# Performance work log

Hardware: AMD Instinct MI355X
Metric: run time of the kernel (lower is better)

Reference implementation:

```python
import jax, jax.numpy as jnp
import numpy as np

B, S, H = 2, 2048, 2048
N_HEADS = 16
HEAD_DIM = H // N_HEADS


def setup_inputs() -> dict:
    key = jax.random.key(0)
    ks = jax.random.split(key, 9)
    s = 1.0 / np.sqrt(H)
    inp = {
        "x": jax.random.normal(ks[0], (B, S, H), dtype=jnp.float32),
        "wq": jax.random.uniform(ks[1], (H, H), jnp.float32, -s, s),
        "bq": jnp.zeros((H,), jnp.float32),
        "wk": jax.random.uniform(ks[2], (H, H), jnp.float32, -s, s),
        "bk": jnp.zeros((H,), jnp.float32),
        "wv": jax.random.uniform(ks[3], (H, H), jnp.float32, -s, s),
        "bv": jnp.zeros((H,), jnp.float32),
        "wo": jax.random.uniform(ks[4], (H, H), jnp.float32, -s, s),
        "bo": jnp.zeros((H,), jnp.float32),
    }
    return inp


def reference(x, wq, bq, wk, bk, wv, bv, wo, bo):
    bsz, seq_len, hidden = x.shape
    scale = HEAD_DIM ** -0.5
    # projections -> [b, h, s, d]
    def proj(w, b):
        y = jnp.einsum("bsh,oh->bso", x, w) + b
        return y.reshape(bsz, seq_len, N_HEADS, HEAD_DIM).transpose(0, 2, 1, 3)
    q = proj(wq, bq)
    k = proj(wk, bk)
    v = proj(wv, bv)
    scores = jnp.einsum("bhqd,bhkd->bhqk", q, k) * scale
    causal = jnp.tril(jnp.ones((seq_len, seq_len), dtype=bool))
    scores = jnp.where(causal, scores, -jnp.inf)
    attn = jax.nn.softmax(scores, axis=-1)
    out = jnp.einsum("bhqk,bhkd->bhqd", attn, v)
    out = out.transpose(0, 2, 1, 3).reshape(bsz, seq_len, hidden)
    return jnp.einsum("bsh,oh->bso", out, wo) + bo
```

## Files before the change

kernel.cpp:

```cpp
#include <hip/hip_runtime.h>
#include <hip/hip_bf16.h>
#include <cstdint>
#include <cstddef>

#define BATCH 2
#define S_LEN 2048
#define HID   2048
#define NH    16
#define HD    128
#define ATT_TILES (32 * NH * BATCH)

typedef short bf16x8 __attribute__((ext_vector_type(8)));
typedef float f32x4  __attribute__((ext_vector_type(4)));

__device__ inline unsigned short f2bf(float f) {
    unsigned int u = __float_as_uint(f);
    unsigned int r = (u + 0x7fffu + ((u >> 16) & 1u)) >> 16;
    return (unsigned short)r;
}

__global__ __launch_bounds__(256) void conv_f32_bf16(const float* __restrict__ src,
                                                     unsigned short* __restrict__ dst,
                                                     long n) {
    long i = ((long)blockIdx.x * 256 + threadIdx.x) * 8;
    if (i >= n) return;
    const float4 a = *(const float4*)(src + i);
    const float4 b = *(const float4*)(src + i + 4);
    union { unsigned short u[8]; bf16x8 v; } o;
    o.u[0] = f2bf(a.x); o.u[1] = f2bf(a.y); o.u[2] = f2bf(a.z); o.u[3] = f2bf(a.w);
    o.u[4] = f2bf(b.x); o.u[5] = f2bf(b.y); o.u[6] = f2bf(b.z); o.u[7] = f2bf(b.w);
    *(bf16x8*)(dst + i) = o.v;
}

__global__ __launch_bounds__(256) void conv4_f32_bf16(const float* __restrict__ s0,
                                                      const float* __restrict__ s1,
                                                      const float* __restrict__ s2,
                                                      const float* __restrict__ s3,
                                                      unsigned short* __restrict__ d0,
                                                      unsigned short* __restrict__ d1,
                                                      unsigned short* __restrict__ d2,
                                                      unsigned short* __restrict__ d3,
                                                      long n) {
    const int z = blockIdx.y;
    const float* src = (z == 0) ? s0 : (z == 1) ? s1 : (z == 2) ? s2 : s3;
    unsigned short* dst = (z == 0) ? d0 : (z == 1) ? d1 : (z == 2) ? d2 : d3;
    long i = ((long)blockIdx.x * 256 + threadIdx.x) * 8;
    if (i >= n) return;
    const float4 a = *(const float4*)(src + i);
    const float4 b = *(const float4*)(src + i + 4);
    union { unsigned short u[8]; bf16x8 v; } o;
    o.u[0] = f2bf(a.x); o.u[1] = f2bf(a.y); o.u[2] = f2bf(a.z); o.u[3] = f2bf(a.w);
    o.u[4] = f2bf(b.x); o.u[5] = f2bf(b.y); o.u[6] = f2bf(b.z); o.u[7] = f2bf(b.w);
    *(bf16x8*)(dst + i) = o.v;
}

__global__ void zero_int(int* p) { *p = 0; }

__device__ __forceinline__ void gemm_core(const unsigned short* __restrict__ A,
                                          const unsigned short* __restrict__ Bw,
                                          const float* __restrict__ bias,
                                          void* __restrict__ Cout,
                                          int M, int N, int K, int mode,
                                          int m0, int n0,
                                          unsigned short* Sm) {
    unsigned short* As = Sm;
    unsigned short* Bs = Sm + 4096;
    const int tid = threadIdx.x;
    const int lane = tid & 63;
    const int wave = tid >> 6;
    const int g = lane >> 4, ln = lane & 15;
    const int wm = (wave & 1) * 64, wn = (wave >> 1) * 64;

    f32x4 acc[4][4];
#pragma unroll
    for (int i = 0; i < 4; ++i)
#pragma unroll
        for (int j = 0; j < 4; ++j) acc[i][j] = (f32x4){0.f, 0.f, 0.f, 0.f};

    const int srow = wave * 16 + (lane >> 2);
    const int scol = (((lane & 3) ^ ((lane >> 3) & 3)) * 8);
    const int rxor = (ln >> 1) & 3;

    for (int k0 = 0; k0 < K; k0 += 32) {
#pragma unroll
        for (int c = 0; c < 2; ++c) {
            const unsigned short* ga = A  + (size_t)(m0 + c * 64 + srow) * K + k0 + scol;
            const unsigned short* gb = Bw + (size_t)(n0 + c * 64 + srow) * K + k0 + scol;
            __builtin_amdgcn_global_load_lds(
                (const __attribute__((address_space(1))) void*)ga,
                (__attribute__((address_space(3))) void*)(As + c * 2048 + wave * 512),
                16, 0, 0);
            __builtin_amdgcn_global_load_lds(
                (const __attribute__((address_space(1))) void*)gb,
                (__attribute__((address_space(3))) void*)(Bs + c * 2048 + wave * 512),
                16, 0, 0);
        }
        __syncthreads();
        bf16x8 af[4], bfr[4];
#pragma unroll
        for (int t = 0; t < 4; ++t) {
            af[t]  = *(const bf16x8*)&As[(wm + t * 16 + ln) * 32 + (g ^ rxor) * 8];
            bfr[t] = *(const bf16x8*)&Bs[(wn + t * 16 + ln) * 32 + (g ^ rxor) * 8];
        }
#pragma unroll
        for (int mt = 0; mt < 4; ++mt)
#pragma unroll
            for (int nt = 0; nt < 4; ++nt)
                acc[mt][nt] = __builtin_amdgcn_mfma_f32_16x16x32_bf16(af[mt], bfr[nt], acc[mt][nt], 0, 0, 0);
        __syncthreads();
    }

    if (mode == 1) {
        const int b = m0 >> 11;
        const int sbase = m0 & 2047;
        const int h = n0 >> 7;
#pragma unroll
        for (int p2 = 0; p2 < 2; ++p2) {
            if ((wave >> 1) == p2) {
#pragma unroll
                for (int nt = 0; nt < 4; ++nt) {
                    const int dl = nt * 16 + ln;
                    const float bn = bias[n0 + p2 * 64 + dl];
#pragma unroll
                    for (int mt = 0; mt < 4; ++mt)
#pragma unroll
                        for (int r = 0; r < 4; ++r) {
                            const int sl = wm + mt * 16 + g * 4 + r;
                            const int psc = (sl >> 3) ^ (dl & 15);
                            Sm[dl * 128 + psc * 8 + (sl & 7)] = f2bf(acc[mt][nt][r] + bn);
                        }
                }
            }
            __syncthreads();
            const int dl = tid >> 2;
            const int dd = p2 * 64 + dl;
            unsigned short* dst = (unsigned short*)Cout +
                ((size_t)(b * NH + h) * HD + dd) * S_LEN + sbase;
#pragma unroll
            for (int j = 0; j < 4; ++j) {
                const int sc = (tid & 3) * 4 + j;
                const int psc = sc ^ (dl & 15);
                *(bf16x8*)(dst + sc * 8) = *(const bf16x8*)&Sm[dl * 128 + psc * 8];
            }
            __syncthreads();
        }
        return;
    }

#pragma unroll
    for (int mt = 0; mt < 4; ++mt)
#pragma unroll
        for (int nt = 0; nt < 4; ++nt) {
            const int n = n0 + wn + nt * 16 + ln;
            const float bn = bias[n];
#pragma unroll
            for (int r = 0; r < 4; ++r) {
                const int m = m0 + wm + mt * 16 + g * 4 + r;
                const float v = acc[mt][nt][r] + bn;
                if (mode == 2) {
                    ((float*)Cout)[(size_t)m * N + n] = v;
                } else {
                    const int b = m >> 11, s = m & 2047;
                    const int h = n >> 7, d = n & 127;
                    ((unsigned short*)Cout)[((((size_t)b * NH + h) * S_LEN + s) * HD + d)] = f2bf(v);
                }
            }
        }
}

__global__ __launch_bounds__(256) void gemm_qkv(const unsigned short* __restrict__ A,
                                                const unsigned short* __restrict__ w0,
                                                const unsigned short* __restrict__ w1,
                                                const unsigned short* __restrict__ w2,
                                                const float* __restrict__ b0,
                                                const float* __restrict__ b1,
                                                const float* __restrict__ b2,
                                                void* o0, void* o1, void* o2,
                                                int M, int N, int K) {
    __shared__ __align__(16) unsigned short Sm[8192];
    const int z = blockIdx.z;
    const unsigned short* Bw = (z == 0) ? w0 : (z == 1) ? w1 : w2;
    const float* bias = (z == 0) ? b0 : (z == 1) ? b1 : b2;
    void* Cout = (z == 0) ? o0 : (z == 1) ? o1 : o2;
    const int mode = (z == 2) ? 1 : 0;
    gemm_core(A, Bw, bias, Cout, M, N, K, mode,
              blockIdx.y * 128, blockIdx.x * 128, Sm);
}

__global__ __launch_bounds__(256) void gemm_bt(const unsigned short* __restrict__ A,
                                               const unsigned short* __restrict__ Bw,
                                               const float* __restrict__ bias,
                                               void* __restrict__ Cout,
                                               int M, int N, int K, int mode) {
    __shared__ __align__(16) unsigned short Sm[8192];
    gemm_core(A, Bw, bias, Cout, M, N, K, mode,
              blockIdx.y * 128, blockIdx.x * 128, Sm);
}

__global__ __launch_bounds__(256) void attn_kernel(const unsigned short* __restrict__ Q,
                                                   const unsigned short* __restrict__ Kk,
                                                   const unsigned short* __restrict__ Vt,
                                                   unsigned short* __restrict__ O,
                                                   int* __restrict__ ticket) {
    __shared__ __align__(16) unsigned short Ks[64 * 128];
    __shared__ __align__(16) unsigned short Vs[144 * 64];
    __shared__ __align__(16) unsigned short Pl[4][16 * 72];
    __shared__ int tsh;
    const int tid = threadIdx.x;
    const int lane = tid & 63;
    const int wave = tid >> 6;
    const int g = lane >> 4, ln = lane & 15;
    const float scale2 = 0.08838834764831845f * 1.4426950408889634f;

    for (int i = tid; i < 16 * 64; i += 256) Vs[128 * 64 + i] = 0x3F80;

    const int kcol = ((tid & 15) ^ ((tid >> 4) & 15)) * 8;
    const int vcol = ((tid & 7) ^ ((tid >> 3) & 7)) * 8;

    for (;;) {
        if (tid == 0) tsh = atomicAdd(ticket, 1);
        __syncthreads();
        const int t = tsh;
        if (t >= ATT_TILES) break;
        const int qt = 31 - (t >> 5);
        const int bh = t & 31;
        const int qbase = qt * 64 + wave * 16;

        const unsigned short* Qp = Q  + (size_t)bh * S_LEN * HD;
        const unsigned short* Kp = Kk + (size_t)bh * S_LEN * HD;
        const unsigned short* Vp = Vt + (size_t)bh * HD * S_LEN;

        bf16x8 aq[4];
#pragma unroll
        for (int dc = 0; dc < 4; ++dc)
            aq[dc] = *(const bf16x8*)&Qp[(size_t)(qbase + ln) * HD + dc * 32 + g * 8];

        f32x4 acc[9];
#pragma unroll
        for (int i = 0; i < 9; ++i) acc[i] = (f32x4){0.f, 0.f, 0.f, 0.f};

        for (int kt = 0; kt <= qt; ++kt) {
            const int kb = kt * 64;
#pragma unroll
            for (int i = 0; i < 4; ++i) {
                const unsigned short* gk = Kp + (size_t)(kb + i * 16 + (tid >> 4)) * HD + kcol;
                __builtin_amdgcn_global_load_lds(
                    (const __attribute__((address_space(1))) void*)gk,
                    (__attribute__((address_space(3))) void*)(Ks + i * 2048 + wave * 512),
                    16, 0, 0);
            }
#pragma unroll
            for (int i = 0; i < 4; ++i) {
                const unsigned short* gv = Vp + (size_t)(i * 32 + (tid >> 3)) * S_LEN + kb + vcol;
                __builtin_amdgcn_global_load_lds(
                    (const __attribute__((address_space(1))) void*)gv,
                    (__attribute__((address_space(3))) void*)(Vs + i * 2048 + wave * 512),
                    16, 0, 0);
            }
            __syncthreads();
            f32x4 sc[4];
#pragma unroll
            for (int nc = 0; nc < 4; ++nc) {
                sc[nc] = (f32x4){0.f, 0.f, 0.f, 0.f};
#pragma unroll
                for (int dc = 0; dc < 4; ++dc) {
                    bf16x8 bk = *(const bf16x8*)&Ks[(nc * 16 + ln) * 128 + ((dc * 4 + g) ^ ln) * 8];
                    sc[nc] = __builtin_amdgcn_mfma_f32_16x16x32_bf16(aq[dc], bk, sc[nc], 0, 0, 0);
                }
            }
            const bool diag = (kt == qt);
#pragma unroll
            for (int nc = 0; nc < 4; ++nc)
#pragma unroll
                for (int r = 0; r < 4; ++r) {
                    float pv = __builtin_amdgcn_exp2f(sc[nc][r] * scale2);
                    if (diag && (nc * 16 + ln > wave * 16 + g * 4 + r)) pv = 0.f;
                    Pl[wave][(g * 4 + r) * 72 + nc * 16 + ln] = f2bf(pv);
                }
#pragma unroll
            for (int kc = 0; kc < 2; ++kc) {
                bf16x8 ap = *(const bf16x8*)&Pl[wave][ln * 72 + kc * 32 + g * 8];
#pragma unroll
                for (int d2 = 0; d2 < 9; ++d2) {
                    bf16x8 bv = *(const bf16x8*)&Vs[(d2 * 16 + ln) * 64 + ((kc * 4 + g) ^ (ln & 7)) * 8];
                    acc[d2] = __builtin_amdgcn_mfma_f32_16x16x32_bf16(ap, bv, acc[d2], 0, 0, 0);
                }
            }
            __syncthreads();
        }
        const int b = bh >> 4, h = bh & 15;
        float inv[4];
#pragma unroll
        for (int r = 0; r < 4; ++r) inv[r] = 1.0f / acc[8][r];
#pragma unroll
        for (int d2 = 0; d2 < 8; ++d2)
#pragma unroll
            for (int r = 0; r < 4; ++r) {
                const int row = qbase + g * 4 + r;
                const int col = h * HD + d2 * 16 + ln;
                O[((size_t)b * S_LEN + row) * HID + col] = f2bf(acc[d2][r] * inv[r]);
            }
    }
}

extern "C" void kernel_launch(void* const* d_in, const int* in_sizes, int n_in,
                              void* d_out, int out_size, void* d_ws, size_t ws_size,
                              hipStream_t stream) {
    const float* x  = (const float*)d_in[0];
    const float* wq = (const float*)d_in[1];
    const float* bq = (const float*)d_in[2];
    const float* wk = (const float*)d_in[3];
    const float* bk = (const float*)d_in[4];
    const float* wv = (const float*)d_in[5];
    const float* bv = (const float*)d_in[6];
    const float* wo = (const float*)d_in[7];
    const float* bo = (const float*)d_in[8];
    float* out = (float*)d_out;

    const long nx = (long)BATCH * S_LEN * HID;
    const long nw = (long)HID * HID;

    char* p = (char*)d_ws;
    unsigned short* xb  = (unsigned short*)p; p += nx * 2;
    unsigned short* wqb = (unsigned short*)p; p += nw * 2;
    unsigned short* wkb = (unsigned short*)p; p += nw * 2;
    unsigned short* wvb = (unsigned short*)p; p += nw * 2;
    unsigned short* wob = (unsigned short*)p; p += nw * 2;
    unsigned short* Qb  = (unsigned short*)p; p += nx * 2;
    unsigned short* Kb  = (unsigned short*)p; p += nx * 2;
    unsigned short* Vtb = (unsigned short*)p; p += nx * 2;
    unsigned short* Ob  = (unsigned short*)p; p += nx * 2;
    int* ticket = (int*)p;

    conv_f32_bf16<<<(int)(nx / 8 / 256), 256, 0, stream>>>(x, xb, nx);
    dim3 cgrid((unsigned)(nw / 8 / 256), 4);
    conv4_f32_bf16<<<cgrid, 256, 0, stream>>>(wq, wk, wv, wo, wqb, wkb, wvb, wob, nw);
    zero_int<<<1, 1, 0, stream>>>(ticket);

    const int M = BATCH * S_LEN;
    dim3 qkvgrid(HID / 128, M / 128, 3);
    gemm_qkv<<<qkvgrid, 256, 0, stream>>>(xb, wqb, wkb, wvb, bq, bk, bv,
                                          Qb, Kb, Vtb, M, HID, HID);

    attn_kernel<<<768, 256, 0, stream>>>(Qb, Kb, Vtb, Ob, ticket);

    dim3 ggrid(HID / 128, M / 128);
    gemm_bt<<<ggrid, 256, 0, stream>>>(Ob, wob, bo, out, M, HID, HID, 2);
}
```

Before: 433.5 us.

## Replace 128x128 GEMMs with 256x256 ping-pong pipelined 8-wave GEMM

Replaces the simple 128x128-tile, 4-wave GEMM used for the QKV and output projections with a 256x256-tile, 8-wave kernel. It uses 128 KB of dynamic LDS with double-buffered A/B stages and interleaves async global-to-LDS loads with MFMA phases under barriers and s_setprio. The goal is to raise data reuse per tile and hide load latency behind compute. In exchange it uses much more LDS, launches fewer blocks (128 per projection), hardcodes K=2048 and relies on fragile hand-placed waitcnt/barrier scheduling. The V-transpose epilogue is also widened to 64-bit packed LDS writes.

Result: faster. 400.7 us (-7.5%).

```diff
diff --git a/kernel.cpp b/kernel.cpp
--- a/kernel.cpp
+++ b/kernel.cpp
@@ -8,6 +8,9 @@
 #define HID   2048
 #define NH    16
 #define HD    128
+#define GK    2048
+#define NT    (GK / 64)
+#define NIT   (NT / 2)
 #define ATT_TILES (32 * NH * BATCH)
 
 typedef short bf16x8 __attribute__((ext_vector_type(8)));
@@ -56,145 +59,202 @@
 
 __global__ void zero_int(int* p) { *p = 0; }
 
-__device__ __forceinline__ void gemm_core(const unsigned short* __restrict__ A,
-                                          const unsigned short* __restrict__ Bw,
-                                          const float* __restrict__ bias,
-                                          void* __restrict__ Cout,
-                                          int M, int N, int K, int mode,
-                                          int m0, int n0,
-                                          unsigned short* Sm) {
-    unsigned short* As = Sm;
-    unsigned short* Bs = Sm + 4096;
-    const int tid = threadIdx.x;
+
+#define STAGE(DU, SRC, KT, H) do {                                            \
+    const unsigned short* _s0 = (SRC) + (size_t)((H) * 128) * GK + (KT) * 64; \
+    __builtin_amdgcn_global_load_lds(                                         \
+        (const __attribute__((address_space(1))) void*)_s0,                   \
+        (__attribute__((address_space(3))) void*)(Sm + (DU) + (H) * 8192 + sdst), \
+        16, 0, 0);                                                            \
+    __builtin_amdgcn_global_load_lds(                                         \
+        (const __attribute__((address_space(1))) void*)(_s0 + (size_t)64 * GK), \
+        (__attribute__((address_space(3))) void*)(Sm + (DU) + (H) * 8192 + 4096 + sdst), \
+        16, 0, 0);                                                            \
+} while (0)
+
+#define READ_A(D, HI) do { _Pragma("unroll")                                  \
+    for (int mi = 0; mi < 4; ++mi) {                                          \
+        const int r_ = wm * 128 + (HI) * 64 + mi * 16 + ln;                   \
+        a[mi][0] = *(const bf16x8*)&Sm[(D) * 32768 + r_ * 64 + sw0];          \
+        a[mi][1] = *(const bf16x8*)&Sm[(D) * 32768 + r_ * 64 + sw1];          \
+    } } while (0)
+
+#define READ_B(D, SEL) do { _Pragma("unroll")                                 \
+    for (int ni = 0; ni < 2; ++ni) {                                          \
+        const int r_ = wn * 64 + ((SEL) * 2 + ni) * 16 + ln;                  \
+        b[(SEL)*2+ni][0] = *(const bf16x8*)&Sm[(D) * 32768 + 16384 + r_ * 64 + sw0]; \
+        b[(SEL)*2+ni][1] = *(const bf16x8*)&Sm[(D) * 32768 + 16384 + r_ * 64 + sw1]; \
+    } } while (0)
+
+#define MFMA16(MB, NS) do { _Pragma("unroll")                                 \
+    for (int mi = 0; mi < 4; ++mi) _Pragma("unroll")                          \
+    for (int ni = 0; ni < 2; ++ni) _Pragma("unroll")                          \
+    for (int ks = 0; ks < 2; ++ks)                                            \
+        acc[(MB)+mi][(NS)*2+ni] = __builtin_amdgcn_mfma_f32_16x16x32_bf16(    \
+            a[mi][ks], b[(NS)*2+ni][ks], acc[(MB)+mi][(NS)*2+ni], 0, 0, 0);   \
+} while (0)
+
+#define PH_BEGIN  __builtin_amdgcn_s_barrier();                               \
+                  asm volatile("s_waitcnt lgkmcnt(0)" ::: "memory");          \
+                  __builtin_amdgcn_s_setprio(1)
+#define PH_END    __builtin_amdgcn_s_setprio(0); __builtin_amdgcn_s_barrier()
+#define PH_END_V4 __builtin_amdgcn_s_setprio(0);                              \
+                  asm volatile("s_waitcnt vmcnt(4)" ::: "memory");            \
+                  __builtin_amdgcn_s_barrier()
+
+__device__ __forceinline__ void gemm256_core(const unsigned short* __restrict__ A,
+                                             const unsigned short* __restrict__ Bw,
+                                             const float* __restrict__ bias,
+                                             void* __restrict__ Cout,
+                                             int mode, int M0, int N0,
+                                             unsigned short* Sm) {
+    const int tid  = threadIdx.x;
     const int lane = tid & 63;
     const int wave = tid >> 6;
-    const int g = lane >> 4, ln = lane & 15;
-    const int wm = (wave & 1) * 64, wn = (wave >> 1) * 64;
-
-    f32x4 acc[4][4];
-#pragma unroll
-    for (int i = 0; i < 4; ++i)
+    const int ln = lane & 15, g = lane >> 4;
+    const int wm = wave & 1, wn = wave >> 1;
+
+    const int strow = tid >> 3;
+    const int stcol = (((tid & 7) ^ ((tid >> 3) & 7)) << 3);
+    const unsigned short* gA = A  + (size_t)(M0 + strow) * GK + stcol;
+    const unsigned short* gB = Bw + (size_t)(N0 + strow) * GK + stcol;
+    const int sdst = wave * 512;
+
+    const int sw0 = ((g    ) ^ (ln & 7)) << 3;
+    const int sw1 = ((g + 4) ^ (ln & 7)) << 3;
+
+    f32x4 acc[8][4];
+#pragma unroll
+    for (int i = 0; i < 8; ++i)
 #pragma unroll
         for (int j = 0; j < 4; ++j) acc[i][j] = (f32x4){0.f, 0.f, 0.f, 0.f};
-
-    const int srow = wave * 16 + (lane >> 2);
-    const int scol = (((lane & 3) ^ ((lane >> 3) & 3)) * 8);
-    const int rxor = (ln >> 1) & 3;
-
-    for (int k0 = 0; k0 < K; k0 += 32) {
-#pragma unroll
-        for (int c = 0; c < 2; ++c) {
-            const unsigned short* ga = A  + (size_t)(m0 + c * 64 + srow) * K + k0 + scol;
-            const unsigned short* gb = Bw + (size_t)(n0 + c * 64 + srow) * K + k0 + scol;
-            __builtin_amdgcn_global_load_lds(
-                (const __attribute__((address_space(1))) void*)ga,
-                (__attribute__((address_space(3))) void*)(As + c * 2048 + wave * 512),
-                16, 0, 0);
-            __builtin_amdgcn_global_load_lds(
-                (const __attribute__((address_space(1))) void*)gb,
-                (__attribute__((address_space(3))) void*)(Bs + c * 2048 + wave * 512),
-                16, 0, 0);
+    bf16x8 a[4][2], b[4][2];
+
+    STAGE(0,     gA, 0, 0); STAGE(0,     gA, 0, 1);
+    STAGE(16384, gB, 0, 0); STAGE(16384, gB, 0, 1);
+    STAGE(32768, gA, 1, 0); STAGE(32768, gA, 1, 1);
+    asm volatile("s_waitcnt vmcnt(4)" ::: "memory");
+    __builtin_amdgcn_s_barrier();
+
+    for (int it = 0; it < NIT; ++it) {
+        const int kt1 = 2 * it + 1;
+        const int kt2 = (2 * it + 2 < NT) ? 2 * it + 2 : NT - 1;
+        const int kt3 = (2 * it + 3 < NT) ? 2 * it + 3 : NT - 1;
+        READ_A(0, 0); READ_B(0, 0);
+        STAGE(49152, gB, kt1, 0);
+        PH_BEGIN; MFMA16(0, 0); PH_END;
+        READ_B(0, 1);
+        STAGE(49152, gB, kt1, 1);
+        PH_BEGIN; MFMA16(0, 1); PH_END;
+        READ_A(0, 1);
+        STAGE(16384, gB, kt2, 0);
+        PH_BEGIN; MFMA16(4, 0); PH_END;
+        STAGE(16384, gB, kt2, 1);
+        PH_BEGIN; MFMA16(4, 1); PH_END_V4;
+        READ_A(1, 0); READ_B(1, 0);
+        STAGE(0, gA, kt2, 0);
+        PH_BEGIN; MFMA16(0, 0); PH_END;
+        READ_B(1, 1);
+        STAGE(0, gA, kt2, 1);
+        PH_BEGIN; MFMA16(0, 1); PH_END;
+        READ_A(1, 1);
+        PH_BEGIN; MFMA16(4, 0); PH_END;
+        STAGE(32768, gA, kt3, 0); STAGE(32768, gA, kt3, 1);
+        PH_BEGIN; MFMA16(4, 1); PH_END_V4;
+    }
+    asm volatile("s_waitcnt vmcnt(0)" ::: "memory");
+    __syncthreads();
+
+    if (mode == 0) {
+        const int bb = M0 >> 11;
+        const int sb = M0 & (S_LEN - 1);
+#pragma unroll
+        for (int nf = 0; nf < 4; ++nf) {
+            const int n = N0 + wn * 64 + nf * 16 + ln;
+            const float bn = bias[n];
+            const int h = n >> 7, d = n & (HD - 1);
+            unsigned short* dst = (unsigned short*)Cout +
+                (((size_t)(bb * NH + h) * S_LEN + sb + wm * 128) * HD + d);
+#pragma unroll
+            for (int mf = 0; mf < 8; ++mf)
+#pragma unroll
+                for (int r = 0; r < 4; ++r)
+                    dst[(size_t)(mf * 16 + g * 4 + r) * HD] = f2bf(acc[mf][nf][r] + bn);
         }
-        __syncthreads();
-        bf16x8 af[4], bfr[4];
-#pragma unroll
-        for (int t = 0; t < 4; ++t) {
-            af[t]  = *(const bf16x8*)&As[(wm + t * 16 + ln) * 32 + (g ^ rxor) * 8];
-            bfr[t] = *(const bf16x8*)&Bs[(wn + t * 16 + ln) * 32 + (g ^ rxor) * 8];
+    } else if (mode == 2) {
+        float* dst = (float*)Cout;
+#pragma unroll
+        for (int nf = 0; nf < 4; ++nf) {
+            const int n = N0 + wn * 64 + nf * 16 + ln;
+            const float bn = bias[n];
+#pragma unroll
+            for (int mf = 0; mf < 8; ++mf)
+#pragma unroll
+                for (int r = 0; r < 4; ++r) {
+                    const int m = M0 + wm * 128 + mf * 16 + g * 4 + r;
+                    dst[(size_t)m * HID + n] = acc[mf][nf][r] + bn;
+                }
         }
-#pragma unroll
-        for (int mt = 0; mt < 4; ++mt)
-#pragma unroll
-            for (int nt = 0; nt < 4; ++nt)
-                acc[mt][nt] = __builtin_amdgcn_mfma_f32_16x16x32_bf16(af[mt], bfr[nt], acc[mt][nt], 0, 0, 0);
-        __syncthreads();
-    }
-
-    if (mode == 1) {
-        const int b = m0 >> 11;
-        const int sbase = m0 & 2047;
-        const int h = n0 >> 7;
-#pragma unroll
-        for (int p2 = 0; p2 < 2; ++p2) {
-            if ((wave >> 1) == p2) {
-#pragma unroll
-                for (int nt = 0; nt < 4; ++nt) {
-                    const int dl = nt * 16 + ln;
-                    const float bn = bias[n0 + p2 * 64 + dl];
-#pragma unroll
-                    for (int mt = 0; mt < 4; ++mt)
-#pragma unroll
-                        for (int r = 0; r < 4; ++r) {
-                            const int sl = wm + mt * 16 + g * 4 + r;
-                            const int psc = (sl >> 3) ^ (dl & 15);
-                            Sm[dl * 128 + psc * 8 + (sl & 7)] = f2bf(acc[mt][nt][r] + bn);
-                        }
+    } else {
+        const int bb = M0 >> 11;
+        const int sb = M0 & (S_LEN - 1);
+#pragma unroll
+        for (int p = 0; p < 2; ++p) {
+            if ((wn >> 1) == p) {
+#pragma unroll
+                for (int nf = 0; nf < 4; ++nf) {
+                    const int dl = (wn & 1) * 64 + nf * 16 + ln;
+                    const float bn = bias[N0 + p * 128 + dl];
+#pragma unroll
+                    for (int mf = 0; mf < 8; ++mf) {
+                        const int sl = wm * 128 + mf * 16 + g * 4;
+                        const int cs = (sl >> 3) ^ (dl & 31);
+                        union { unsigned short u[4]; unsigned long long q; } pk;
+#pragma unroll
+                        for (int r = 0; r < 4; ++r) pk.u[r] = f2bf(acc[mf][nf][r] + bn);
+                        *(unsigned long long*)&Sm[dl * 256 + cs * 8 + (sl & 7)] = pk.q;
+                    }
                 }
             }
             __syncthreads();
-            const int dl = tid >> 2;
-            const int dd = p2 * 64 + dl;
-            unsigned short* dst = (unsigned short*)Cout +
-                ((size_t)(b * NH + h) * HD + dd) * S_LEN + sbase;
-#pragma unroll
-            for (int j = 0; j < 4; ++j) {
-                const int sc = (tid & 3) * 4 + j;
-                const int psc = sc ^ (dl & 15);
-                *(bf16x8*)(dst + sc * 8) = *(const bf16x8*)&Sm[dl * 128 + psc * 8];
+            {
+                const int dl = tid >> 2;
+                const int h = (N0 >> 7) + p;
+                unsigned short* dst = (unsigned short*)Cout +
+                    ((size_t)(bb * NH + h) * HD + dl) * S_LEN + sb;
+#pragma unroll
+                for (int jj = 0; jj < 8; ++jj) {
+                    const int sc = (tid & 3) + jj * 4;
+                    const int cs = sc ^ (dl & 31);
+                    *(bf16x8*)(dst + sc * 8) = *(const bf16x8*)&Sm[dl * 256 + cs * 8];
+                }
             }
             __syncthreads();
         }
-        return;
     }
-
-#pragma unroll
-    for (int mt = 0; mt < 4; ++mt)
-#pragma unroll
-        for (int nt = 0; nt < 4; ++nt) {
-            const int n = n0 + wn + nt * 16 + ln;
-            const float bn = bias[n];
-#pragma unroll
-            for (int r = 0; r < 4; ++r) {
-                const int m = m0 + wm + mt * 16 + g * 4 + r;
-                const float v = acc[mt][nt][r] + bn;
-                if (mode == 2) {
-                    ((float*)Cout)[(size_t)m * N + n] = v;
-                } else {
-                    const int b = m >> 11, s = m & 2047;
-                    const int h = n >> 7, d = n & 127;
-                    ((unsigned short*)Cout)[((((size_t)b * NH + h) * S_LEN + s) * HD + d)] = f2bf(v);
-                }
-            }
-        }
-}
-
-__global__ __launch_bounds__(256) void gemm_qkv(const unsigned short* __restrict__ A,
-                                                const unsigned short* __restrict__ w0,
-                                                const unsigned short* __restrict__ w1,
-                                                const unsigned short* __restrict__ w2,
-                                                const float* __restrict__ b0,
-                                                const float* __restrict__ b1,
-                                                const float* __restrict__ b2,
-                                                void* o0, void* o1, void* o2,
-                                                int M, int N, int K) {
-    __shared__ __align__(16) unsigned short Sm[8192];
+}
+
+__global__ __launch_bounds__(512, 2) void gemm_qkv256(
+        const unsigned short* __restrict__ A,
+        const unsigned short* __restrict__ w0, const unsigned short* __restrict__ w1,
+        const unsigned short* __restrict__ w2,
+        const float* __restrict__ b0, const float* __restrict__ b1,
+        const float* __restrict__ b2,
+        void* o0, void* o1, void* o2) {
+    extern __shared__ __align__(16) unsigned short Sm[];
     const int z = blockIdx.z;
     const unsigned short* Bw = (z == 0) ? w0 : (z == 1) ? w1 : w2;
     const float* bias = (z == 0) ? b0 : (z == 1) ? b1 : b2;
     void* Cout = (z == 0) ? o0 : (z == 1) ? o1 : o2;
-    const int mode = (z == 2) ? 1 : 0;
-    gemm_core(A, Bw, bias, Cout, M, N, K, mode,
-              blockIdx.y * 128, blockIdx.x * 128, Sm);
-}
-
-__global__ __launch_bounds__(256) void gemm_bt(const unsigned short* __restrict__ A,
-                                               const unsigned short* __restrict__ Bw,
-                                               const float* __restrict__ bias,
-                                               void* __restrict__ Cout,
-                                               int M, int N, int K, int mode) {
-    __shared__ __align__(16) unsigned short Sm[8192];
-    gemm_core(A, Bw, bias, Cout, M, N, K, mode,
-              blockIdx.y * 128, blockIdx.x * 128, Sm);
+    gemm256_core(A, Bw, bias, Cout, (z == 2) ? 1 : 0,
+                 blockIdx.y * 256, blockIdx.x * 256, Sm);
+}
+
+__global__ __launch_bounds__(512, 2) void gemm_out256(
+        const unsigned short* __restrict__ A, const unsigned short* __restrict__ Bw,
+        const float* __restrict__ bias, float* __restrict__ Cout) {
+    extern __shared__ __align__(16) unsigned short Sm[];
+    gemm256_core(A, Bw, bias, Cout, 2, blockIdx.y * 256, blockIdx.x * 256, Sm);
 }
 
 __global__ __launch_bounds__(256) void attn_kernel(const unsigned short* __restrict__ Q,
@@ -338,12 +398,12 @@
     zero_int<<<1, 1, 0, stream>>>(ticket);
 
     const int M = BATCH * S_LEN;
-    dim3 qkvgrid(HID / 128, M / 128, 3);
-    gemm_qkv<<<qkvgrid, 256, 0, stream>>>(xb, wqb, wkb, wvb, bq, bk, bv,
-                                          Qb, Kb, Vtb, M, HID, HID);
+    dim3 qkvgrid(HID / 256, M / 256, 3);
+    gemm_qkv256<<<qkvgrid, 512, 131072, stream>>>(xb, wqb, wkb, wvb, bq, bk, bv,
+                                                  Qb, Kb, Vtb);
 
     attn_kernel<<<768, 256, 0, stream>>>(Qb, Kb, Vtb, Ob, ticket);
 
-    dim3 ggrid(HID / 128, M / 128);
-    gemm_bt<<<ggrid, 256, 0, stream>>>(Ob, wob, bo, out, M, HID, HID, 2);
-}
+    dim3 ogrid(HID / 256, M / 256);
+    gemm_out256<<<ogrid, 512, 131072, stream>>>(Ob, wob, bo, out);
+}
```
